# Performance work log

Hardware: AMD Instinct MI355X
Metric: run time of the kernel (lower is better)

## Reference

```python
import jax, jax.numpy as jnp
import numpy as np

B, N, C_IN, C_OUT, E_DIM = 16, 1024, 64, 64, 4


def setup_inputs() -> dict:
    key = jax.random.key(0)
    ks = jax.random.split(key, 7)
    x = jax.random.normal(ks[0], (B, N, C_IN), dtype=jnp.float32)
    adj = jax.random.uniform(ks[1], (B, N, N), dtype=jnp.float32)
    edge_attr = jax.random.randint(ks[2], (B, N, N, 1), 0, E_DIM, dtype=jnp.int32)
    scale = 1.0 / np.sqrt(C_IN)
    W_rel = jax.random.normal(ks[3], (C_IN, C_OUT), dtype=jnp.float32) * scale
    b_rel = jax.random.normal(ks[4], (C_OUT,), dtype=jnp.float32) * scale
    W_root = jax.random.normal(ks[5], (C_IN, C_OUT), dtype=jnp.float32) * scale
    w_edge = jax.random.normal(ks[6], (E_DIM,), dtype=jnp.float32)
    return {"x": x, "adj": adj, "edge_attr": edge_attr,
            "W_rel": W_rel, "b_rel": b_rel, "W_root": W_root, "w_edge": w_edge}


def reference(x, adj, edge_attr, W_rel, b_rel, W_root, w_edge):
    # one_hot(edge_attr) @ w_edge == gather of w_edge by edge type (same math,
    # avoids materializing the B x N x N x E_DIM one-hot tensor).
    e = w_edge[edge_attr[..., 0]]            # [B, N, N]
    adj_w = adj * e                           # weighted adjacency
    out = jnp.matmul(adj_w, x)                # [B, N, C_IN] aggregation (aggr='add')
    out = jnp.matmul(out, W_rel) + b_rel      # lin_rel
    out = out + jnp.matmul(x, W_root)         # lin_root (no bias)
    return out
```

## Files before the change

kernel.cpp:

```cpp
#include <hip/hip_runtime.h>

#define BB 16
#define NN 1024
#define CC 64

typedef __attribute__((ext_vector_type(8))) short short8;
typedef __attribute__((ext_vector_type(4))) float f32x4;
typedef __attribute__((ext_vector_type(4))) int   i32x4;

typedef __attribute__((address_space(3))) void lds_void_t;
typedef const __attribute__((address_space(1))) void gbl_void_t;

__device__ __forceinline__ void load_lds16(const void* g, void* l) {
    __builtin_amdgcn_global_load_lds((gbl_void_t*)g, (lds_void_t*)l, 16, 0, 0);
}

__device__ __forceinline__ unsigned short bf16_rne(float f) {
    unsigned u = __float_as_uint(f);
    u += 0x7fffu + ((u >> 16) & 1u);
    return (unsigned short)(u >> 16);
}

extern "C" __global__ __launch_bounds__(256)
void precompute(const float* __restrict__ x, const float* __restrict__ W_rel,
                const float* __restrict__ W_root, const float* __restrict__ b_rel,
                unsigned short* __restrict__ xw_sw, float* __restrict__ out)
{
    __shared__ float wrel_s[64 * 64];
    __shared__ float wroot_s[64 * 64];
    __shared__ float x_s[16 * 68];

    const int t = threadIdx.x;
    #pragma unroll
    for (int k = 0; k < 4; ++k) {
        int i4 = t + 256 * k;
        ((float4*)wrel_s)[i4]  = ((const float4*)W_rel)[i4];
        ((float4*)wroot_s)[i4] = ((const float4*)W_root)[i4];
    }
    const int row0 = blockIdx.x * 16;
    {
        int r = t >> 4, c4 = t & 15;
        *(float4*)(x_s + r * 68 + c4 * 4) = ((const float4*)(x + (size_t)(row0 + r) * CC))[c4];
    }
    __syncthreads();

    const int c4 = t & 15;
    const int r  = t >> 4;
    float aw0 = 0.f, aw1 = 0.f, aw2 = 0.f, aw3 = 0.f;
    float ar0 = 0.f, ar1 = 0.f, ar2 = 0.f, ar3 = 0.f;
    const float* xrow = x_s + r * 68;
    #pragma unroll 8
    for (int k = 0; k < 64; ++k) {
        float xv = xrow[k];
        float4 wv = ((const float4*)(wrel_s  + k * 64))[c4];
        float4 rv = ((const float4*)(wroot_s + k * 64))[c4];
        aw0 += xv * wv.x; aw1 += xv * wv.y; aw2 += xv * wv.z; aw3 += xv * wv.w;
        ar0 += xv * rv.x; ar1 += xv * rv.y; ar2 += xv * rv.z; ar3 += xv * rv.w;
    }

    const int row_g = row0 + r;
    {
        const float4 bv = ((const float4*)b_rel)[c4];
        ((float4*)out)[(size_t)row_g * 16 + c4] =
            make_float4(ar0 + bv.x, ar1 + bv.y, ar2 + bv.z, ar3 + bv.w);
    }
    {
        const int b = row_g >> 10;
        const int k = row_g & 1023;
        const int kb = k >> 5;
        const int qk = (k >> 3) & 3;
        const int j  = k & 7;
        const int c  = 4 * c4;
        const int n0 = c >> 4;
        const int n  = c & 15;
        size_t off = ((size_t)b << 16) + (size_t)((kb * 4 + n0) << 9)
                   + (size_t)((n + (qk << 4)) << 3) + j;
        xw_sw[off]      = bf16_rne(aw0);
        xw_sw[off + 8]  = bf16_rne(aw1);
        xw_sw[off + 16] = bf16_rne(aw2);
        xw_sw[off + 24] = bf16_rne(aw3);
    }
}

#define ADJ_OFF 0
#define EA_OFF  16384
#define XW_OFF  32768

extern "C" __global__ __launch_bounds__(256, 3)
void gnn_mfma(const float* __restrict__ adj, const int* __restrict__ ea,
              const float* __restrict__ w_edge,
              const unsigned short* __restrict__ xw_sw,
              float* __restrict__ out)
{
    __shared__ __align__(16) char lds[49152];

    const int t    = threadIdx.x;
    const int w    = t >> 6;
    const int lane = t & 63;
    const int m    = lane & 15;
    const int q    = lane >> 4;
    const int wm   = w >> 1;
    const int wk   = w & 1;

    const int mtile = blockIdx.x & 31;
    const int kh    = (blockIdx.x >> 5) & 1;
    const int b     = blockIdx.x >> 6;
    const int row0  = mtile << 5;

    const float w0 = w_edge[0], w1 = w_edge[1], w2 = w_edge[2], w3 = w_edge[3];
    const float d1 = w1 - w0;
    const float d2 = w2 - 2.f * w1 + w0;
    const float d3 = w3 - 3.f * w2 + 3.f * w1 - w0;
    const float c3 = d3 * (1.f / 6.f);
    const float c2 = 0.5f * d2 - 0.5f * d3;
    const float c1 = d1 - 0.5f * d2 + (1.f / 3.f) * d3;
    const float c0 = w0;

    const size_t bbase = ((size_t)b << 20);
    const unsigned short* xwb = xw_sw + ((size_t)b << 16);

    f32x4 acc0 = {0.f, 0.f, 0.f, 0.f};
    f32x4 acc1 = acc0, acc2 = acc0, acc3 = acc0;

    for (int c = 0; c < 4; ++c) {
        const int kc = (kh << 9) + (c << 7);
        if (c) __syncthreads();

        #pragma unroll
        for (int f = w; f < 16; f += 4) {
            int mh = f >> 3;
            int kb = (f >> 1) & 3;
            int h  = f & 1;
            int row = row0 + (mh << 4) + m;
            int k   = kc + (kb << 5) + (q << 3) + (h << 2);
            size_t goff = bbase + ((size_t)row << 10) + k;
            int doff = ((mh * 4 + kb) << 11) + (h << 10);
            load_lds16(adj + goff, lds + ADJ_OFF + doff);
            load_lds16(ea  + goff, lds + EA_OFF  + doff);
        }
        #pragma unroll
        for (int f = w; f < 16; f += 4) {
            int kb = f >> 2, n0 = f & 3;
            int kbg = (kh << 4) + (c << 2) + kb;
            load_lds16(xwb + (((kbg << 2) + n0) << 9) + (lane << 3),
                       lds + XW_OFF + (f << 10));
        }
        __syncthreads();

        #pragma unroll
        for (int s = 0; s < 2; ++s) {
            int kb = (wk << 1) + s;
            int fbase = ((wm * 4 + kb) << 11) + (lane << 4);
            f32x4 alo = *(const f32x4*)(lds + ADJ_OFF + fbase);
            f32x4 ahi = *(const f32x4*)(lds + ADJ_OFF + fbase + 1024);
            i32x4 elo = *(const i32x4*)(lds + EA_OFF + fbase);
            i32x4 ehi = *(const i32x4*)(lds + EA_OFF + fbase + 1024);

            #define WSEL(ev) __builtin_fmaf(__builtin_fmaf(__builtin_fmaf(c3, (float)(ev), c2), (float)(ev), c1), (float)(ev), c0)
            float p0 = alo[0] * WSEL(elo[0]);
            float p1 = alo[1] * WSEL(elo[1]);
            float p2 = alo[2] * WSEL(elo[2]);
            float p3 = alo[3] * WSEL(elo[3]);
            float p4 = ahi[0] * WSEL(ehi[0]);
            float p5 = ahi[1] * WSEL(ehi[1]);
            float p6 = ahi[2] * WSEL(ehi[2]);
            float p7 = ahi[3] * WSEL(ehi[3]);
            #undef WSEL

            union { int i[4]; short8 s8; } af;
            af.i[0] = __builtin_amdgcn_perm(__float_as_uint(p1), __float_as_uint(p0), 0x07060302u);
            af.i[1] = __builtin_amdgcn_perm(__float_as_uint(p3), __float_as_uint(p2), 0x07060302u);
            af.i[2] = __builtin_amdgcn_perm(__float_as_uint(p5), __float_as_uint(p4), 0x07060302u);
            af.i[3] = __builtin_amdgcn_perm(__float_as_uint(p7), __float_as_uint(p6), 0x07060302u);

            const char* xbase = lds + XW_OFF + ((kb << 2) << 10) + (lane << 4);
            short8 bf0 = *(const short8*)(xbase);
            short8 bf1 = *(const short8*)(xbase + 1024);
            short8 bf2 = *(const short8*)(xbase + 2048);
            short8 bf3 = *(const short8*)(xbase + 3072);

            acc0 = __builtin_amdgcn_mfma_f32_16x16x32_bf16(af.s8, bf0, acc0, 0, 0, 0);
            acc1 = __builtin_amdgcn_mfma_f32_16x16x32_bf16(af.s8, bf1, acc1, 0, 0, 0);
            acc2 = __builtin_amdgcn_mfma_f32_16x16x32_bf16(af.s8, bf2, acc2, 0, 0, 0);
            acc3 = __builtin_amdgcn_mfma_f32_16x16x32_bf16(af.s8, bf3, acc3, 0, 0, 0);
        }
    }

    __syncthreads();
    float* scratch = (float*)lds;
    if (wk == 1) {
        float* buf = scratch + wm * 1088;
        #pragma unroll
        for (int rg = 0; rg < 4; ++rg) {
            int rbase = (q * 4 + rg) * 68 + m;
            buf[rbase]      = acc0[rg];
            buf[rbase + 16] = acc1[rg];
            buf[rbase + 32] = acc2[rg];
            buf[rbase + 48] = acc3[rg];
        }
    }
    __syncthreads();
    if (wk == 0) {
        const float* buf = scratch + wm * 1088;
        float* obase = out + (((size_t)b << 10) + row0 + (wm << 4)) * 64;
        #pragma unroll
        for (int rg = 0; rg < 4; ++rg) {
            int rpad = (q * 4 + rg) * 68 + m;
            int rout = (q * 4 + rg) * 64 + m;
            #pragma unroll
            for (int n0 = 0; n0 < 4; ++n0) {
                float v = (n0 == 0 ? acc0[rg] : n0 == 1 ? acc1[rg] : n0 == 2 ? acc2[rg] : acc3[rg]);
                v += buf[rpad + n0 * 16];
                atomicAdd(obase + rout + n0 * 16, v);
            }
        }
    }
}

extern "C" void kernel_launch(void* const* d_in, const int* in_sizes, int n_in,
                              void* d_out, int out_size, void* d_ws, size_t ws_size,
                              hipStream_t stream) {
    const float* x      = (const float*)d_in[0];
    const float* adj    = (const float*)d_in[1];
    const int*   ea     = (const int*)  d_in[2];
    const float* W_rel  = (const float*)d_in[3];
    const float* b_rel  = (const float*)d_in[4];
    const float* W_root = (const float*)d_in[5];
    const float* w_edge = (const float*)d_in[6];
    float* out = (float*)d_out;

    unsigned short* xw_sw = (unsigned short*)d_ws;

    precompute<<<BB * NN / 16, 256, 0, stream>>>(x, W_rel, W_root, b_rel, xw_sw, out);
    gnn_mfma<<<BB * (NN / 32) * 2, 256, 0, stream>>>(adj, ea, w_edge, xw_sw, out);
}
```

Baseline: 170.9 us.

## Double-buffer LDS staging with smaller K chunks to overlap loads with MFMA

```diff
diff --git a/kernel.cpp b/kernel.cpp
--- a/kernel.cpp
+++ b/kernel.cpp
@@ -82,9 +82,7 @@
     }
 }
 
-#define ADJ_OFF 0
-#define EA_OFF  16384
-#define XW_OFF  32768
+#define CHUNK_B 24576
 
 extern "C" __global__ __launch_bounds__(256, 3)
 void gnn_mfma(const float* __restrict__ adj, const int* __restrict__ ea,
@@ -92,7 +90,7 @@
               const unsigned short* __restrict__ xw_sw,
               float* __restrict__ out)
 {
-    __shared__ __align__(16) char lds[49152];
+    __shared__ __align__(16) char lds[2 * CHUNK_B];
 
     const int t    = threadIdx.x;
     const int w    = t >> 6;
@@ -122,39 +120,48 @@
     f32x4 acc0 = {0.f, 0.f, 0.f, 0.f};
     f32x4 acc1 = acc0, acc2 = acc0, acc3 = acc0;
 
-    for (int c = 0; c < 4; ++c) {
-        const int kc = (kh << 9) + (c << 7);
-        if (c) __syncthreads();
-
-        #pragma unroll
-        for (int f = w; f < 16; f += 4) {
-            int mh = f >> 3;
-            int kb = (f >> 1) & 3;
-            int h  = f & 1;
-            int row = row0 + (mh << 4) + m;
-            int k   = kc + (kb << 5) + (q << 3) + (h << 2);
-            size_t goff = bbase + ((size_t)row << 10) + k;
-            int doff = ((mh * 4 + kb) << 11) + (h << 10);
-            load_lds16(adj + goff, lds + ADJ_OFF + doff);
-            load_lds16(ea  + goff, lds + EA_OFF  + doff);
-        }
-        #pragma unroll
-        for (int f = w; f < 16; f += 4) {
-            int kb = f >> 2, n0 = f & 3;
-            int kbg = (kh << 4) + (c << 2) + kb;
-            load_lds16(xwb + (((kbg << 2) + n0) << 9) + (lane << 3),
-                       lds + XW_OFF + (f << 10));
-        }
-        __syncthreads();
-
-        #pragma unroll
-        for (int s = 0; s < 2; ++s) {
-            int kb = (wk << 1) + s;
-            int fbase = ((wm * 4 + kb) << 11) + (lane << 4);
-            f32x4 alo = *(const f32x4*)(lds + ADJ_OFF + fbase);
-            f32x4 ahi = *(const f32x4*)(lds + ADJ_OFF + fbase + 1024);
-            i32x4 elo = *(const i32x4*)(lds + EA_OFF + fbase);
-            i32x4 ehi = *(const i32x4*)(lds + EA_OFF + fbase + 1024);
+    #define STAGE(c)                                                            \
+    {                                                                           \
+        const int buf = ((c) & 1) * CHUNK_B;                                    \
+        const int kc  = (kh << 9) + ((c) << 6);                                 \
+        _Pragma("unroll")                                                       \
+        for (int r = 0; r < 2; ++r) {                                           \
+            int f  = w + (r << 2);                                    \
+            int mh = f >> 2, kb = (f >> 1) & 1, h = f & 1;                      \
+            int row = row0 + (mh << 4) + m;                                     \
+            int k   = kc + (kb << 5) + (q << 3) + (h << 2);                     \
+            size_t goff = bbase + ((size_t)row << 10) + k;                      \
+            int doff = buf + (((mh << 1) + kb) << 11) + (h << 10);              \
+            load_lds16(adj + goff, lds + doff);                                 \
+            load_lds16(ea  + goff, lds + 8192 + doff);                          \
+        }                                                                       \
+        _Pragma("unroll")                                                       \
+        for (int r = 0; r < 2; ++r) {                                           \
+            int f  = w + (r << 2);                                              \
+            int kb = f >> 2, n0 = f & 3;                                        \
+            int kbg = (kh << 4) + ((c) << 1) + kb;                              \
+            load_lds16(xwb + (((kbg << 2) + n0) << 9) + (lane << 3),            \
+                       lds + buf + 16384 + (f << 10));                          \
+        }                                                                       \
+    }
+
+    STAGE(0);
+
+    #pragma unroll
+    for (int c = 0; c < 8; ++c) {
+        if (c < 7) STAGE(c + 1);
+
+        if (c < 7) asm volatile("s_waitcnt vmcnt(6)\n\ts_barrier" ::: "memory");
+        else       asm volatile("s_waitcnt vmcnt(0)\n\ts_barrier" ::: "memory");
+
+        {
+            const int buf  = (c & 1) * CHUNK_B;
+            const int frag = (wm << 1) + wk;
+            const char* ab = lds + buf + (frag << 11) + (lane << 4);
+            f32x4 alo = *(const f32x4*)(ab);
+            f32x4 ahi = *(const f32x4*)(ab + 1024);
+            i32x4 elo = *(const i32x4*)(ab + 8192);
+            i32x4 ehi = *(const i32x4*)(ab + 8192 + 1024);
 
             #define WSEL(ev) __builtin_fmaf(__builtin_fmaf(__builtin_fmaf(c3, (float)(ev), c2), (float)(ev), c1), (float)(ev), c0)
             float p0 = alo[0] * WSEL(elo[0]);
@@ -173,7 +180,7 @@
             af.i[2] = __builtin_amdgcn_perm(__float_as_uint(p5), __float_as_uint(p4), 0x07060302u);
             af.i[3] = __builtin_amdgcn_perm(__float_as_uint(p7), __float_as_uint(p6), 0x07060302u);
 
-            const char* xbase = lds + XW_OFF + ((kb << 2) << 10) + (lane << 4);
+            const char* xbase = lds + buf + 16384 + ((wk << 2) << 10) + (lane << 4);
             short8 bf0 = *(const short8*)(xbase);
             short8 bf1 = *(const short8*)(xbase + 1024);
             short8 bf2 = *(const short8*)(xbase + 2048);
@@ -184,7 +191,10 @@
             acc2 = __builtin_amdgcn_mfma_f32_16x16x32_bf16(af.s8, bf2, acc2, 0, 0, 0);
             acc3 = __builtin_amdgcn_mfma_f32_16x16x32_bf16(af.s8, bf3, acc3, 0, 0, 0);
         }
-    }
+
+        if (c < 6) asm volatile("s_waitcnt lgkmcnt(0)\n\ts_barrier" ::: "memory");
+    }
+    #undef STAGE
 
     __syncthreads();
     float* scratch = (float*)lds;
```

New measurement: 171.7 us. No clear change (+0.5%).

## Convert adjacency to bf16 at load time and split K within block

Applied to the files above, without the earlier changes.

```diff
diff --git a/kernel.cpp b/kernel.cpp
--- a/kernel.cpp
+++ b/kernel.cpp
@@ -6,7 +6,6 @@
 
 typedef __attribute__((ext_vector_type(8))) short short8;
 typedef __attribute__((ext_vector_type(4))) float f32x4;
-typedef __attribute__((ext_vector_type(4))) int   i32x4;
 
 typedef __attribute__((address_space(3))) void lds_void_t;
 typedef const __attribute__((address_space(1))) void gbl_void_t;
@@ -82,9 +81,8 @@
     }
 }
 
-#define ADJ_OFF 0
-#define EA_OFF  16384
-#define XW_OFF  32768
+#define AW_STR  528
+#define XW_OFF_L 16896
 
 extern "C" __global__ __launch_bounds__(256, 3)
 void gnn_mfma(const float* __restrict__ adj, const int* __restrict__ ea,
@@ -92,19 +90,18 @@
               const unsigned short* __restrict__ xw_sw,
               float* __restrict__ out)
 {
-    __shared__ __align__(16) char lds[49152];
+    __shared__ __align__(16) char lds[49664];
 
     const int t    = threadIdx.x;
     const int w    = t >> 6;
     const int lane = t & 63;
     const int m    = lane & 15;
     const int q    = lane >> 4;
-    const int wm   = w >> 1;
-    const int wk   = w & 1;
+    const int mf   = w & 1;
+    const int kh   = w >> 1;
 
     const int mtile = blockIdx.x & 31;
-    const int kh    = (blockIdx.x >> 5) & 1;
-    const int b     = blockIdx.x >> 6;
+    const int b     = blockIdx.x >> 5;
     const int row0  = mtile << 5;
 
     const float w0 = w_edge[0], w1 = w_edge[1], w2 = w_edge[2], w3 = w_edge[3];
@@ -116,80 +113,61 @@
     const float c1 = d1 - 0.5f * d2 + (1.f / 3.f) * d3;
     const float c0 = w0;
 
-    const size_t bbase = ((size_t)b << 20);
-    const unsigned short* xwb = xw_sw + ((size_t)b << 16);
+    const size_t growbase = ((size_t)b << 10) + row0;
+    const char*  xwb = (const char*)xw_sw + ((size_t)b << 17);
 
     f32x4 acc0 = {0.f, 0.f, 0.f, 0.f};
     f32x4 acc1 = acc0, acc2 = acc0, acc3 = acc0;
 
+    #pragma unroll 1
     for (int c = 0; c < 4; ++c) {
-        const int kc = (kh << 9) + (c << 7);
         if (c) __syncthreads();
 
         #pragma unroll
-        for (int f = w; f < 16; f += 4) {
-            int mh = f >> 3;
-            int kb = (f >> 1) & 3;
-            int h  = f & 1;
-            int row = row0 + (mh << 4) + m;
-            int k   = kc + (kb << 5) + (q << 3) + (h << 2);
-            size_t goff = bbase + ((size_t)row << 10) + k;
-            int doff = ((mh * 4 + kb) << 11) + (h << 10);
-            load_lds16(adj + goff, lds + ADJ_OFF + doff);
-            load_lds16(ea  + goff, lds + EA_OFF  + doff);
-        }
-        #pragma unroll
-        for (int f = w; f < 16; f += 4) {
-            int kb = f >> 2, n0 = f & 3;
-            int kbg = (kh << 4) + (c << 2) + kb;
-            load_lds16(xwb + (((kbg << 2) + n0) << 9) + (lane << 3),
-                       lds + XW_OFF + (f << 10));
+        for (int r = 0; r < 8; ++r) {
+            const int row = (w << 3) + r;
+            const size_t g = ((growbase + row) << 10) + (c << 8) + (lane << 2);
+            float4 av = *(const float4*)(adj + g);
+            int4   ev = *(const int4*)  (ea  + g);
+            #define WSEL(e) __builtin_fmaf(__builtin_fmaf(__builtin_fmaf(c3, (float)(e), c2), (float)(e), c1), (float)(e), c0)
+            float p0 = av.x * WSEL(ev.x);
+            float p1 = av.y * WSEL(ev.y);
+            float p2 = av.z * WSEL(ev.z);
+            float p3 = av.w * WSEL(ev.w);
+            #undef WSEL
+            uint2 pk;
+            pk.x = __builtin_amdgcn_perm(__float_as_uint(p1), __float_as_uint(p0), 0x07060302u);
+            pk.y = __builtin_amdgcn_perm(__float_as_uint(p3), __float_as_uint(p2), 0x07060302u);
+            *(uint2*)(lds + row * AW_STR + (lane << 3)) = pk;
+        }
+        #pragma unroll
+        for (int r = 0; r < 8; ++r) {
+            const int i = (w << 3) + r;
+            const int off = (i << 10) + (lane << 4);
+            load_lds16(xwb + (c << 15) + off, lds + XW_OFF_L + off);
         }
         __syncthreads();
 
         #pragma unroll
-        for (int s = 0; s < 2; ++s) {
-            int kb = (wk << 1) + s;
-            int fbase = ((wm * 4 + kb) << 11) + (lane << 4);
-            f32x4 alo = *(const f32x4*)(lds + ADJ_OFF + fbase);
-            f32x4 ahi = *(const f32x4*)(lds + ADJ_OFF + fbase + 1024);
-            i32x4 elo = *(const i32x4*)(lds + EA_OFF + fbase);
-            i32x4 ehi = *(const i32x4*)(lds + EA_OFF + fbase + 1024);
-
-            #define WSEL(ev) __builtin_fmaf(__builtin_fmaf(__builtin_fmaf(c3, (float)(ev), c2), (float)(ev), c1), (float)(ev), c0)
-            float p0 = alo[0] * WSEL(elo[0]);
-            float p1 = alo[1] * WSEL(elo[1]);
-            float p2 = alo[2] * WSEL(elo[2]);
-            float p3 = alo[3] * WSEL(elo[3]);
-            float p4 = ahi[0] * WSEL(ehi[0]);
-            float p5 = ahi[1] * WSEL(ehi[1]);
-            float p6 = ahi[2] * WSEL(ehi[2]);
-            float p7 = ahi[3] * WSEL(ehi[3]);
-            #undef WSEL
-
-            union { int i[4]; short8 s8; } af;
-            af.i[0] = __builtin_amdgcn_perm(__float_as_uint(p1), __float_as_uint(p0), 0x07060302u);
-            af.i[1] = __builtin_amdgcn_perm(__float_as_uint(p3), __float_as_uint(p2), 0x07060302u);
-            af.i[2] = __builtin_amdgcn_perm(__float_as_uint(p5), __float_as_uint(p4), 0x07060302u);
-            af.i[3] = __builtin_amdgcn_perm(__float_as_uint(p7), __float_as_uint(p6), 0x07060302u);
-
-            const char* xbase = lds + XW_OFF + ((kb << 2) << 10) + (lane << 4);
-            short8 bf0 = *(const short8*)(xbase);
-            short8 bf1 = *(const short8*)(xbase + 1024);
-            short8 bf2 = *(const short8*)(xbase + 2048);
-            short8 bf3 = *(const short8*)(xbase + 3072);
-
-            acc0 = __builtin_amdgcn_mfma_f32_16x16x32_bf16(af.s8, bf0, acc0, 0, 0, 0);
-            acc1 = __builtin_amdgcn_mfma_f32_16x16x32_bf16(af.s8, bf1, acc1, 0, 0, 0);
-            acc2 = __builtin_amdgcn_mfma_f32_16x16x32_bf16(af.s8, bf2, acc2, 0, 0, 0);
-            acc3 = __builtin_amdgcn_mfma_f32_16x16x32_bf16(af.s8, bf3, acc3, 0, 0, 0);
+        for (int s = 0; s < 4; ++s) {
+            const int kb = (kh << 2) + s;
+            short8 afr = *(const short8*)(lds + ((mf << 4) + m) * AW_STR + (kb << 6) + (q << 4));
+            const char* xb = lds + XW_OFF_L + (kb << 12) + (lane << 4);
+            short8 bf0 = *(const short8*)(xb);
+            short8 bf1 = *(const short8*)(xb + 1024);
+            short8 bf2 = *(const short8*)(xb + 2048);
+            short8 bf3 = *(const short8*)(xb + 3072);
+            acc0 = __builtin_amdgcn_mfma_f32_16x16x32_bf16(afr, bf0, acc0, 0, 0, 0);
+            acc1 = __builtin_amdgcn_mfma_f32_16x16x32_bf16(afr, bf1, acc1, 0, 0, 0);
+            acc2 = __builtin_amdgcn_mfma_f32_16x16x32_bf16(afr, bf2, acc2, 0, 0, 0);
+            acc3 = __builtin_amdgcn_mfma_f32_16x16x32_bf16(afr, bf3, acc3, 0, 0, 0);
         }
     }
 
     __syncthreads();
     float* scratch = (float*)lds;
-    if (wk == 1) {
-        float* buf = scratch + wm * 1088;
+    if (kh == 1) {
+        float* buf = scratch + mf * 1088;
         #pragma unroll
         for (int rg = 0; rg < 4; ++rg) {
             int rbase = (q * 4 + rg) * 68 + m;
@@ -200,9 +178,9 @@
         }
     }
     __syncthreads();
-    if (wk == 0) {
-        const float* buf = scratch + wm * 1088;
-        float* obase = out + (((size_t)b << 10) + row0 + (wm << 4)) * 64;
+    if (kh == 0) {
+        const float* buf = scratch + mf * 1088;
+        float* obase = out + (growbase + (mf << 4)) * 64;
         #pragma unroll
         for (int rg = 0; rg < 4; ++rg) {
             int rpad = (q * 4 + rg) * 68 + m;
@@ -211,7 +189,7 @@
             for (int n0 = 0; n0 < 4; ++n0) {
                 float v = (n0 == 0 ? acc0[rg] : n0 == 1 ? acc1[rg] : n0 == 2 ? acc2[rg] : acc3[rg]);
                 v += buf[rpad + n0 * 16];
-                atomicAdd(obase + rout + n0 * 16, v);
+                obase[rout + n0 * 16] += v;
             }
         }
     }
@@ -232,5 +210,5 @@
     unsigned short* xw_sw = (unsigned short*)d_ws;
 
     precompute<<<BB * NN / 16, 256, 0, stream>>>(x, W_rel, W_root, b_rel, xw_sw, out);
-    gnn_mfma<<<BB * (NN / 32) * 2, 256, 0, stream>>>(adj, ea, w_edge, xw_sw, out);
-}
+    gnn_mfma<<<BB * (NN / 32), 256, 0, stream>>>(adj, ea, w_edge, xw_sw, out);
+}
```

Result: no change. 171.6 us (+0.4%).

## Warp-specialize aggregation kernel with triple-buffered producer/consumer LDS pipeline

Applied to the files above, without the earlier changes.

```diff
diff --git a/kernel.cpp b/kernel.cpp
--- a/kernel.cpp
+++ b/kernel.cpp
@@ -82,30 +82,29 @@
     }
 }
 
-#define ADJ_OFF 0
+#define SLOT_B  40960
 #define EA_OFF  16384
 #define XW_OFF  32768
 
-extern "C" __global__ __launch_bounds__(256, 3)
+extern "C" __global__ __launch_bounds__(1024, 4)
 void gnn_mfma(const float* __restrict__ adj, const int* __restrict__ ea,
               const float* __restrict__ w_edge,
               const unsigned short* __restrict__ xw_sw,
               float* __restrict__ out)
 {
-    __shared__ __align__(16) char lds[49152];
+    __shared__ __align__(16) char lds[3 * SLOT_B];
 
     const int t    = threadIdx.x;
     const int w    = t >> 6;
     const int lane = t & 63;
     const int m    = lane & 15;
     const int q    = lane >> 4;
-    const int wm   = w >> 1;
-    const int wk   = w & 1;
-
-    const int mtile = blockIdx.x & 31;
-    const int kh    = (blockIdx.x >> 5) & 1;
-    const int b     = blockIdx.x >> 6;
-    const int row0  = mtile << 5;
+
+    const int mtile = blockIdx.x & 15;
+    const int b     = blockIdx.x >> 4;
+    const int row0  = mtile << 6;
+    const size_t growbase = ((size_t)b << 10) + row0;
+    const char*  xwb = (const char*)xw_sw + ((size_t)b << 17);
 
     const float w0 = w_edge[0], w1 = w_edge[1], w2 = w_edge[2], w3 = w_edge[3];
     const float d1 = w1 - w0;
@@ -116,45 +115,52 @@
     const float c1 = d1 - 0.5f * d2 + (1.f / 3.f) * d3;
     const float c0 = w0;
 
-    const size_t bbase = ((size_t)b << 20);
-    const unsigned short* xwb = xw_sw + ((size_t)b << 16);
+    const bool producer = (w < 8);
+    const int cw = w - 8;
+    const int mf = cw & 3;
+    const int kh = cw >> 2;
 
     f32x4 acc0 = {0.f, 0.f, 0.f, 0.f};
     f32x4 acc1 = acc0, acc2 = acc0, acc3 = acc0;
 
-    for (int c = 0; c < 4; ++c) {
-        const int kc = (kh << 9) + (c << 7);
-        if (c) __syncthreads();
-
-        #pragma unroll
-        for (int f = w; f < 16; f += 4) {
-            int mh = f >> 3;
-            int kb = (f >> 1) & 3;
-            int h  = f & 1;
-            int row = row0 + (mh << 4) + m;
-            int k   = kc + (kb << 5) + (q << 3) + (h << 2);
-            size_t goff = bbase + ((size_t)row << 10) + k;
-            int doff = ((mh * 4 + kb) << 11) + (h << 10);
-            load_lds16(adj + goff, lds + ADJ_OFF + doff);
-            load_lds16(ea  + goff, lds + EA_OFF  + doff);
-        }
-        #pragma unroll
-        for (int f = w; f < 16; f += 4) {
-            int kb = f >> 2, n0 = f & 3;
-            int kbg = (kh << 4) + (c << 2) + kb;
-            load_lds16(xwb + (((kbg << 2) + n0) << 9) + (lane << 3),
-                       lds + XW_OFF + (f << 10));
-        }
-        __syncthreads();
-
-        #pragma unroll
-        for (int s = 0; s < 2; ++s) {
-            int kb = (wk << 1) + s;
-            int fbase = ((wm * 4 + kb) << 11) + (lane << 4);
-            f32x4 alo = *(const f32x4*)(lds + ADJ_OFF + fbase);
-            f32x4 ahi = *(const f32x4*)(lds + ADJ_OFF + fbase + 1024);
-            i32x4 elo = *(const i32x4*)(lds + EA_OFF + fbase);
-            i32x4 ehi = *(const i32x4*)(lds + EA_OFF + fbase + 1024);
+    #define ISSUE(c, s)                                                          \
+    {                                                                            \
+        char* slot = lds + (s) * SLOT_B;                                         \
+        const int pmf = w >> 1, pkb = w & 1;                                     \
+        const size_t rowb = ((growbase + (pmf << 4) + m) << 10) + ((c) << 6)     \
+                          + (pkb << 5) + (q << 3);                               \
+        char* adst = slot + (w << 11) + (lane << 4);                             \
+        load_lds16(adj + rowb,                adst);                             \
+        load_lds16(adj + rowb + 4,            adst + 1024);                      \
+        load_lds16(ea  + rowb,                adst + EA_OFF);                    \
+        load_lds16(ea  + rowb + 4,            adst + EA_OFF + 1024);             \
+        load_lds16(xwb + ((c) << 13) + (w << 10) + (lane << 4),                  \
+                   slot + XW_OFF + (w << 10) + (lane << 4));                     \
+    }
+
+    if (producer) {
+        ISSUE(0, 0);
+        ISSUE(1, 1);
+        asm volatile("s_waitcnt vmcnt(5)" ::: "memory");
+    }
+    asm volatile("s_barrier" ::: "memory");
+
+    int sc = 0;
+    int sp = 2;
+    #pragma unroll 1
+    for (int c = 0; c < 16; ++c) {
+        if (producer) {
+            if (c + 2 < 16) ISSUE(c + 2, sp);
+            if (c < 14) asm volatile("s_waitcnt vmcnt(5)" ::: "memory");
+            else        asm volatile("s_waitcnt vmcnt(0)" ::: "memory");
+        } else {
+            const char* slot = lds + sc * SLOT_B;
+            const int tile = (mf << 1) + kh;
+            const char* ab = slot + (tile << 11) + (lane << 4);
+            f32x4 alo = *(const f32x4*)(ab);
+            f32x4 ahi = *(const f32x4*)(ab + 1024);
+            i32x4 elo = *(const i32x4*)(ab + EA_OFF);
+            i32x4 ehi = *(const i32x4*)(ab + EA_OFF + 1024);
 
             #define WSEL(ev) __builtin_fmaf(__builtin_fmaf(__builtin_fmaf(c3, (float)(ev), c2), (float)(ev), c1), (float)(ev), c0)
             float p0 = alo[0] * WSEL(elo[0]);
@@ -173,23 +179,27 @@
             af.i[2] = __builtin_amdgcn_perm(__float_as_uint(p5), __float_as_uint(p4), 0x07060302u);
             af.i[3] = __builtin_amdgcn_perm(__float_as_uint(p7), __float_as_uint(p6), 0x07060302u);
 
-            const char* xbase = lds + XW_OFF + ((kb << 2) << 10) + (lane << 4);
-            short8 bf0 = *(const short8*)(xbase);
-            short8 bf1 = *(const short8*)(xbase + 1024);
-            short8 bf2 = *(const short8*)(xbase + 2048);
-            short8 bf3 = *(const short8*)(xbase + 3072);
+            const char* xb = slot + XW_OFF + (kh << 12) + (lane << 4);
+            short8 bf0 = *(const short8*)(xb);
+            short8 bf1 = *(const short8*)(xb + 1024);
+            short8 bf2 = *(const short8*)(xb + 2048);
+            short8 bf3 = *(const short8*)(xb + 3072);
 
             acc0 = __builtin_amdgcn_mfma_f32_16x16x32_bf16(af.s8, bf0, acc0, 0, 0, 0);
             acc1 = __builtin_amdgcn_mfma_f32_16x16x32_bf16(af.s8, bf1, acc1, 0, 0, 0);
             acc2 = __builtin_amdgcn_mfma_f32_16x16x32_bf16(af.s8, bf2, acc2, 0, 0, 0);
             acc3 = __builtin_amdgcn_mfma_f32_16x16x32_bf16(af.s8, bf3, acc3, 0, 0, 0);
         }
-    }
+        asm volatile("s_barrier" ::: "memory");
+        sc = (sc == 2) ? 0 : sc + 1;
+        sp = (sp == 2) ? 0 : sp + 1;
+    }
+    #undef ISSUE
 
     __syncthreads();
     float* scratch = (float*)lds;
-    if (wk == 1) {
-        float* buf = scratch + wm * 1088;
+    if (!producer && kh == 1) {
+        float* buf = scratch + mf * 1088;
         #pragma unroll
         for (int rg = 0; rg < 4; ++rg) {
             int rbase = (q * 4 + rg) * 68 + m;
@@ -200,9 +210,9 @@
         }
     }
     __syncthreads();
-    if (wk == 0) {
-        const float* buf = scratch + wm * 1088;
-        float* obase = out + (((size_t)b << 10) + row0 + (wm << 4)) * 64;
+    if (!producer && kh == 0) {
+        const float* buf = scratch + mf * 1088;
+        float* obase = out + (growbase + (mf << 4)) * 64;
         #pragma unroll
         for (int rg = 0; rg < 4; ++rg) {
             int rpad = (q * 4 + rg) * 68 + m;
@@ -211,7 +221,7 @@
             for (int n0 = 0; n0 < 4; ++n0) {
                 float v = (n0 == 0 ? acc0[rg] : n0 == 1 ? acc1[rg] : n0 == 2 ? acc2[rg] : acc3[rg]);
                 v += buf[rpad + n0 * 16];
-                atomicAdd(obase + rout + n0 * 16, v);
+                obase[rout + n0 * 16] += v;
             }
         }
     }
@@ -232,5 +242,5 @@
     unsigned short* xw_sw = (unsigned short*)d_ws;
 
     precompute<<<BB * NN / 16, 256, 0, stream>>>(x, W_rel, W_root, b_rel, xw_sw, out);
-    gnn_mfma<<<BB * (NN / 32) * 2, 256, 0, stream>>>(adj, ea, w_edge, xw_sw, out);
-}
+    gnn_mfma<<<BB * (NN / 64), 1024, 0, stream>>>(adj, ea, w_edge, xw_sw, out);
+}
```

Measured after the change: 179.0 us. 4.7% more time.
